# Kernel optimization log

Hardware: AMD Instinct MI355X
Metric: run time of the kernel (lower is better)

## Reference

```python
import jax, jax.numpy as jnp
import numpy as np

QMAX = 127.0          # int8 clip bound (symmetric, preserve-zero)
QDIV = 127.5          # AQT int8 scale divisor: 2**(bits-1) - 0.5


def _safe(s):
    # avoid div-by-zero for all-zero rows/cols
    return jnp.where(s == 0.0, 1.0, s)


def setup_inputs() -> dict:
    key = jax.random.key(0)
    k1, k2 = jax.random.split(key)
    lhs = jax.random.normal(k1, (8192, 4096), dtype=jnp.float32)
    rhs = jax.random.normal(k2, (4096, 4096), dtype=jnp.float32)
    return {"lhs": lhs, "rhs": rhs}


def reference(lhs, rhs):
    # --- dynamic symmetric int8 quantization (AQT abs-max calibration) ---
    # lhs: contract over axis 1 -> per-row scale [M, 1]
    s_l = _safe(jnp.max(jnp.abs(lhs), axis=1, keepdims=True) / QDIV)
    # rhs: contract over axis 0 -> per-column scale [1, N]
    s_r = _safe(jnp.max(jnp.abs(rhs), axis=0, keepdims=True) / QDIV)

    q_l = jnp.clip(jnp.round(lhs / s_l), -QMAX, QMAX).astype(jnp.int8)
    q_r = jnp.clip(jnp.round(rhs / s_r), -QMAX, QMAX).astype(jnp.int8)

    # --- integer matmul with int32 accumulation ---
    acc = jax.lax.dot_general(
        q_l, q_r,
        dimension_numbers=(((1,), (0,)), ((), ())),
        preferred_element_type=jnp.int32,
    )

    # --- dequantize: outer product of per-row / per-column scales ---
    return acc.astype(jnp.float32) * s_l * s_r
```

## Files before the change

kernel.cpp:

```cpp
#include <hip/hip_runtime.h>
#include <stdint.h>

#define M_DIM 8192
#define N_DIM 4096
#define K_DIM 4096
#define QMAXF 127.0f
#define QDIVF 127.5f

typedef int v4i __attribute__((ext_vector_type(4)));

typedef __attribute__((address_space(3))) void lds_void_t;
typedef __attribute__((address_space(1))) const void glb_void_t;

static __device__ __forceinline__ void load_lds16(const void* g, void* l) {
    __builtin_amdgcn_global_load_lds((glb_void_t*)g, (lds_void_t*)l, 16, 0, 0);
}

__global__ __launch_bounds__(256) void row_quant_kernel(
        const float* __restrict__ lhs, float* __restrict__ sL,
        int8_t* __restrict__ ql) {
    const int row = blockIdx.x;
    const float4* rp = (const float4*)(lhs + (size_t)row * K_DIM);
    const int t = threadIdx.x;
    float4 v[4];
    float m = 0.0f;
#pragma unroll
    for (int i = 0; i < 4; ++i) {
        v[i] = rp[t + i * 256];
        m = fmaxf(m, fmaxf(fmaxf(fabsf(v[i].x), fabsf(v[i].y)),
                           fmaxf(fabsf(v[i].z), fabsf(v[i].w))));
    }
#pragma unroll
    for (int off = 32; off; off >>= 1) m = fmaxf(m, __shfl_down(m, off, 64));
    __shared__ float wmax[4];
    if ((t & 63) == 0) wmax[t >> 6] = m;
    __syncthreads();
    const float mm = fmaxf(fmaxf(wmax[0], wmax[1]), fmaxf(wmax[2], wmax[3]));
    float s = mm / QDIVF;
    s = (s == 0.0f) ? 1.0f : s;
    if (t == 0) sL[row] = s;
    unsigned* qo = (unsigned*)ql + (size_t)row * 1024;
#pragma unroll
    for (int i = 0; i < 4; ++i) {
        int q0 = (int)fminf(fmaxf(rintf(v[i].x / s), -QMAXF), QMAXF);
        int q1 = (int)fminf(fmaxf(rintf(v[i].y / s), -QMAXF), QMAXF);
        int q2 = (int)fminf(fmaxf(rintf(v[i].z / s), -QMAXF), QMAXF);
        int q3 = (int)fminf(fmaxf(rintf(v[i].w / s), -QMAXF), QMAXF);
        qo[t + i * 256] = (q0 & 255) | ((q1 & 255) << 8) | ((q2 & 255) << 16)
                        | ((unsigned)(q3 & 255) << 24);
    }
}

__global__ __launch_bounds__(256) void col_absmax_kernel(
        const float* __restrict__ rhs, unsigned* __restrict__ bits) {
    const int col = blockIdx.x * 256 + threadIdx.x;
    const int r0 = blockIdx.y * 64;
    float m = 0.0f;
#pragma unroll 4
    for (int r = 0; r < 64; ++r)
        m = fmaxf(m, fabsf(rhs[(size_t)(r0 + r) * N_DIM + col]));
    atomicMax(&bits[col], __float_as_uint(m));
}

__global__ __launch_bounds__(256) void col_scale_kernel(
        const unsigned* __restrict__ bits, float* __restrict__ sR) {
    const int c = blockIdx.x * 256 + threadIdx.x;
    float s = __uint_as_float(bits[c]) / QDIVF;
    sR[c] = (s == 0.0f) ? 1.0f : s;
}

__global__ __launch_bounds__(256) void quant_rhs_t_kernel(
        const float* __restrict__ rhs, const float* __restrict__ sR,
        int8_t* __restrict__ qbT) {
    __shared__ __align__(16) int8_t lt[64][80];
    const int n0 = blockIdx.x * 64;
    const int k0 = blockIdx.y * 64;
    const int t = threadIdx.x;
    const int nloc = t & 63;
    const int kq = (t >> 6) * 16;
    const float s = sR[n0 + nloc];
#pragma unroll
    for (int i = 0; i < 4; ++i) {
        unsigned pack = 0;
#pragma unroll
        for (int j = 0; j < 4; ++j) {
            int kk = kq + i * 4 + j;
            float x = rhs[(size_t)(k0 + kk) * N_DIM + n0 + nloc];
            int q = (int)fminf(fmaxf(rintf(x / s), -QMAXF), QMAXF);
            pack |= (unsigned)(q & 255) << (8 * j);
        }
        *(unsigned*)&lt[nloc][kq + i * 4] = pack;
    }
    __syncthreads();
    const int nn = t >> 2, ch = t & 3;
    v4i val = *(const v4i*)&lt[nn][ch * 16];
    *(v4i*)&qbT[(size_t)(n0 + nn) * K_DIM + k0 + ch * 16] = val;
}


#define BAR() do { asm volatile("" ::: "memory");          \
                   __builtin_amdgcn_s_barrier();           \
                   asm volatile("" ::: "memory"); } while (0)

#define VMCNT(N) asm volatile("s_waitcnt vmcnt(%0)" :: "n"(N) : "memory")

#define STAGE_A(h, kt, bq) \
    load_lds16(gA0 + (size_t)((h) * 128) * K_DIM + (size_t)(kt) * 64, \
               lds + (bq) * 16384 + (h) * 8192 + sdst)
#define STAGE_B(h, kt, bq) \
    load_lds16(gB0 + (size_t)((h) * 128) * K_DIM + (size_t)(kt) * 64, \
               lds + 65536 + (bq) * 16384 + (h) * 8192 + sdst)

#define RD_A(BUF, MM) (*(const v4i*)(lds + (BUF) * 16384 + aoff[MM]))
#define RD_B(BUF, NN) (*(const v4i*)(lds + (BUF) * 16384 + boff[NN]))

#define TILE(KT, BUF, P, S, VM, RDN) do {                                       \
    _Pragma("unroll") for (int nn = 0; nn < 4; ++nn)                            \
        bfII[nn] = RD_B(BUF, 4 + nn);                                           \
    if (S) { STAGE_A(0, (KT) + 3, ((BUF) + 3) & 3);                             \
             STAGE_A(1, (KT) + 3, ((BUF) + 3) & 3);                             \
             STAGE_B(0, (KT) + 3, ((BUF) + 3) & 3);                             \
             STAGE_B(1, (KT) + 3, ((BUF) + 3) & 3); }                           \
    __builtin_amdgcn_s_setprio(1);                                              \
    _Pragma("unroll") for (int mm = 0; mm < 4; ++mm)                            \
    _Pragma("unroll") for (int nn = 0; nn < 4; ++nn)                            \
        acc[mm][nn] = __builtin_amdgcn_mfma_i32_16x16x64_i8(                    \
            af[P][mm], bfI[P][nn], acc[mm][nn], 0, 0, 0);                       \
    __builtin_amdgcn_s_setprio(0);                                              \
    if (RDN) {                                                                  \
        _Pragma("unroll") for (int mm = 0; mm < 4; ++mm)                        \
            af[(P) ^ 1][mm] = RD_A(((BUF) + 1) & 3, mm);                        \
        _Pragma("unroll") for (int nn = 0; nn < 4; ++nn)                        \
            bfI[(P) ^ 1][nn] = RD_B(((BUF) + 1) & 3, nn);                       \
    }                                                                           \
    __builtin_amdgcn_s_setprio(1);                                              \
    _Pragma("unroll") for (int mm = 0; mm < 4; ++mm)                            \
    _Pragma("unroll") for (int nn = 0; nn < 4; ++nn)                            \
        acc[mm][4 + nn] = __builtin_amdgcn_mfma_i32_16x16x64_i8(                \
            af[P][mm], bfII[nn], acc[mm][4 + nn], 0, 0, 0);                     \
    __builtin_amdgcn_s_setprio(0);                                              \
    VMCNT(VM);                                                                  \
    BAR();                                                                      \
} while (0)

__global__ __launch_bounds__(512, 2) void gemm_i8_kernel(
        const int8_t* __restrict__ qa, const int8_t* __restrict__ qbT,
        const float* __restrict__ sL, const float* __restrict__ sR,
        float* __restrict__ out) {
    __shared__ __align__(16) int8_t lds[131072];

    const int t = threadIdx.x;
    const int wave = t >> 6;
    const int lane = t & 63;

    const int bid = blockIdx.x;
    const int swz = (bid & 7) * 64 + (bid >> 3);
    const int brow = (swz & 31) * 256;
    const int bcol = (swz >> 5) * 256;

    const int wm = (wave >> 1) * 64;
    const int wn = (wave & 1) * 128;

    int aoff[4], boff[8];
#pragma unroll
    for (int m = 0; m < 4; ++m) {
        int row = wm + m * 16 + (lane & 15);
        aoff[m] = row * 64 + (((lane >> 4) ^ ((row >> 1) & 3)) * 16);
    }
#pragma unroll
    for (int n = 0; n < 8; ++n) {
        int row = wn + n * 16 + (lane & 15);
        boff[n] = 65536 + row * 64 + (((lane >> 4) ^ ((row >> 1) & 3)) * 16);
    }

    v4i acc[4][8];
#pragma unroll
    for (int m = 0; m < 4; ++m)
#pragma unroll
        for (int n = 0; n < 8; ++n) acc[m][n] = (v4i){0, 0, 0, 0};

    const int srow = t >> 2;
    const int lc = (t & 3) ^ ((srow >> 1) & 3);
    const int8_t* gA0 = qa  + (size_t)(brow + srow) * K_DIM + lc * 16;
    const int8_t* gB0 = qbT + (size_t)(bcol + srow) * K_DIM + lc * 16;
    const int sdst = t * 16;

    v4i af[2][4], bfI[2][4], bfII[4];

    STAGE_A(0, 0, 0); STAGE_A(1, 0, 0); STAGE_B(0, 0, 0); STAGE_B(1, 0, 0);
    STAGE_A(0, 1, 1); STAGE_A(1, 1, 1); STAGE_B(0, 1, 1); STAGE_B(1, 1, 1);
    STAGE_A(0, 2, 2); STAGE_A(1, 2, 2); STAGE_B(0, 2, 2); STAGE_B(1, 2, 2);
    VMCNT(4);
    BAR();
#pragma unroll
    for (int mm = 0; mm < 4; ++mm) af[0][mm] = RD_A(0, mm);
#pragma unroll
    for (int nn = 0; nn < 4; ++nn) bfI[0][nn] = RD_B(0, nn);

    for (int kt = 0; kt < 60; kt += 4) {
        TILE(kt + 0, 0, 0, 1, 4, 1);
        TILE(kt + 1, 1, 1, 1, 4, 1);
        TILE(kt + 2, 2, 0, 1, 4, 1);
        TILE(kt + 3, 3, 1, 1, 4, 1);
    }
    TILE(60, 0, 0, 1, 4, 1);
    TILE(61, 1, 1, 0, 0, 1);
    TILE(62, 2, 0, 0, 0, 1);
    TILE(63, 3, 1, 0, 0, 0);

    const int r4 = (lane >> 4) * 4;
    const int cc = lane & 15;
#pragma unroll
    for (int m = 0; m < 4; ++m) {
        const int grow0 = brow + wm + m * 16 + r4;
        const float s0 = sL[grow0 + 0];
        const float s1 = sL[grow0 + 1];
        const float s2 = sL[grow0 + 2];
        const float s3 = sL[grow0 + 3];
#pragma unroll
        for (int n = 0; n < 8; ++n) {
            const int gcol = bcol + wn + n * 16 + cc;
            const float sc = sR[gcol];
            float* o = out + (size_t)grow0 * N_DIM + gcol;
            o[0 * N_DIM] = (float)acc[m][n][0] * s0 * sc;
            o[1 * N_DIM] = (float)acc[m][n][1] * s1 * sc;
            o[2 * N_DIM] = (float)acc[m][n][2] * s2 * sc;
            o[3 * N_DIM] = (float)acc[m][n][3] * s3 * sc;
        }
    }
}

extern "C" void kernel_launch(void* const* d_in, const int* in_sizes, int n_in,
                              void* d_out, int out_size, void* d_ws, size_t ws_size,
                              hipStream_t stream) {
    const float* lhs = (const float*)d_in[0];
    const float* rhs = (const float*)d_in[1];
    float* out = (float*)d_out;

    uint8_t* ws = (uint8_t*)d_ws;
    int8_t* ql    = (int8_t*)ws;
    int8_t* qbT   = (int8_t*)(ws + 33554432);
    float* sL     = (float*)(ws + 50331648);
    float* sR     = (float*)(ws + 50331648 + 32768);
    unsigned* bits = (unsigned*)(ws + 50331648 + 32768 + 16384);

    hipMemsetAsync(bits, 0, N_DIM * sizeof(unsigned), stream);

    row_quant_kernel<<<M_DIM, 256, 0, stream>>>(lhs, sL, ql);
    col_absmax_kernel<<<dim3(N_DIM / 256, K_DIM / 64), 256, 0, stream>>>(rhs, bits);
    col_scale_kernel<<<N_DIM / 256, 256, 0, stream>>>(bits, sR);
    quant_rhs_t_kernel<<<dim3(N_DIM / 64, K_DIM / 64), 256, 0, stream>>>(rhs, sR, qbT);
    gemm_i8_kernel<<<dim3(M_DIM / 256 * N_DIM / 256), 512, 0, stream>>>(ql, qbT, sL, sR, out);
}
```

Before: 220.2 us.

## Shrink GEMM tile to 256x128 with double-buffered LDS and higher occupancy

Replaces the 256x256 block tile with a 4-stage LDS pipeline by a 256x128 tile using only two LDS buffers (48KB) and a simpler load-then-compute loop that waits for all loads each K step. Launch bounds are raised to allow four blocks per CU, and the XCD-aware block swizzle is rewritten for the new grid shape. The aim is to hide latency through occupancy rather than software pipelining. The smaller tile lowers arithmetic intensity and the full vmcnt(0) wait exposes global load latency each iteration.

```diff
diff --git a/kernel.cpp b/kernel.cpp
--- a/kernel.cpp
+++ b/kernel.cpp
@@ -104,109 +104,93 @@
 
 #define VMCNT(N) asm volatile("s_waitcnt vmcnt(%0)" :: "n"(N) : "memory")
 
-#define STAGE_A(h, kt, bq) \
-    load_lds16(gA0 + (size_t)((h) * 128) * K_DIM + (size_t)(kt) * 64, \
-               lds + (bq) * 16384 + (h) * 8192 + sdst)
-#define STAGE_B(h, kt, bq) \
-    load_lds16(gB0 + (size_t)((h) * 128) * K_DIM + (size_t)(kt) * 64, \
-               lds + 65536 + (bq) * 16384 + (h) * 8192 + sdst)
-
 #define RD_A(BUF, MM) (*(const v4i*)(lds + (BUF) * 16384 + aoff[MM]))
-#define RD_B(BUF, NN) (*(const v4i*)(lds + (BUF) * 16384 + boff[NN]))
-
-#define TILE(KT, BUF, P, S, VM, RDN) do {                                       \
-    _Pragma("unroll") for (int nn = 0; nn < 4; ++nn)                            \
-        bfII[nn] = RD_B(BUF, 4 + nn);                                           \
-    if (S) { STAGE_A(0, (KT) + 3, ((BUF) + 3) & 3);                             \
-             STAGE_A(1, (KT) + 3, ((BUF) + 3) & 3);                             \
-             STAGE_B(0, (KT) + 3, ((BUF) + 3) & 3);                             \
-             STAGE_B(1, (KT) + 3, ((BUF) + 3) & 3); }                           \
+#define RD_B(BUF, NN) (*(const v4i*)(lds + 32768 + (BUF) * 8192 + boff[NN]))
+
+#define TILE(BUF, S) do {                                                       \
+    if (S) {                                                                    \
+        load_lds16(pA,                      lds + ((BUF) ^ 1) * 16384 + sdst);  \
+        load_lds16(pA + (size_t)128 * K_DIM,                                    \
+                   lds + ((BUF) ^ 1) * 16384 + 8192 + sdst);                    \
+        load_lds16(pB, lds + 32768 + ((BUF) ^ 1) * 8192 + sdst);                \
+        pA += 64; pB += 64;                                                     \
+    }                                                                           \
+    _Pragma("unroll") for (int mm = 0; mm < 4; ++mm) af[mm] = RD_A(BUF, mm);    \
+    _Pragma("unroll") for (int nn = 0; nn < 4; ++nn) bf[nn] = RD_B(BUF, nn);    \
     __builtin_amdgcn_s_setprio(1);                                              \
     _Pragma("unroll") for (int mm = 0; mm < 4; ++mm)                            \
     _Pragma("unroll") for (int nn = 0; nn < 4; ++nn)                            \
         acc[mm][nn] = __builtin_amdgcn_mfma_i32_16x16x64_i8(                    \
-            af[P][mm], bfI[P][nn], acc[mm][nn], 0, 0, 0);                       \
+            af[mm], bf[nn], acc[mm][nn], 0, 0, 0);                              \
     __builtin_amdgcn_s_setprio(0);                                              \
-    if (RDN) {                                                                  \
-        _Pragma("unroll") for (int mm = 0; mm < 4; ++mm)                        \
-            af[(P) ^ 1][mm] = RD_A(((BUF) + 1) & 3, mm);                        \
-        _Pragma("unroll") for (int nn = 0; nn < 4; ++nn)                        \
-            bfI[(P) ^ 1][nn] = RD_B(((BUF) + 1) & 3, nn);                       \
-    }                                                                           \
-    __builtin_amdgcn_s_setprio(1);                                              \
-    _Pragma("unroll") for (int mm = 0; mm < 4; ++mm)                            \
-    _Pragma("unroll") for (int nn = 0; nn < 4; ++nn)                            \
-        acc[mm][4 + nn] = __builtin_amdgcn_mfma_i32_16x16x64_i8(                \
-            af[P][mm], bfII[nn], acc[mm][4 + nn], 0, 0, 0);                     \
-    __builtin_amdgcn_s_setprio(0);                                              \
-    VMCNT(VM);                                                                  \
+    VMCNT(0);                                                                   \
     BAR();                                                                      \
 } while (0)
 
-__global__ __launch_bounds__(512, 2) void gemm_i8_kernel(
+__global__ __launch_bounds__(512, 4) void gemm_i8_kernel(
         const int8_t* __restrict__ qa, const int8_t* __restrict__ qbT,
         const float* __restrict__ sL, const float* __restrict__ sR,
         float* __restrict__ out) {
-    __shared__ __align__(16) int8_t lds[131072];
+    __shared__ __align__(16) int8_t lds[49152];
 
     const int t = threadIdx.x;
     const int wave = t >> 6;
     const int lane = t & 63;
 
     const int bid = blockIdx.x;
-    const int swz = (bid & 7) * 64 + (bid >> 3);
-    const int brow = (swz & 31) * 256;
-    const int bcol = (swz >> 5) * 256;
+    const int xcd = bid & 7;
+    const int idx = bid >> 3;
+    const int mt = (xcd >> 1) * 8 + (idx & 7);
+    const int nt = (xcd & 1) * 16 + (idx >> 3);
+    const int brow = mt * 256;
+    const int bcol = nt * 128;
 
     const int wm = (wave >> 1) * 64;
-    const int wn = (wave & 1) * 128;
-
-    int aoff[4], boff[8];
+    const int wn = (wave & 1) * 64;
+
+    int aoff[4], boff[4];
 #pragma unroll
     for (int m = 0; m < 4; ++m) {
         int row = wm + m * 16 + (lane & 15);
         aoff[m] = row * 64 + (((lane >> 4) ^ ((row >> 1) & 3)) * 16);
     }
 #pragma unroll
-    for (int n = 0; n < 8; ++n) {
+    for (int n = 0; n < 4; ++n) {
         int row = wn + n * 16 + (lane & 15);
-        boff[n] = 65536 + row * 64 + (((lane >> 4) ^ ((row >> 1) & 3)) * 16);
-    }
-
-    v4i acc[4][8];
+        boff[n] = row * 64 + (((lane >> 4) ^ ((row >> 1) & 3)) * 16);
+    }
+
+    v4i acc[4][4];
 #pragma unroll
     for (int m = 0; m < 4; ++m)
 #pragma unroll
-        for (int n = 0; n < 8; ++n) acc[m][n] = (v4i){0, 0, 0, 0};
+        for (int n = 0; n < 4; ++n) acc[m][n] = (v4i){0, 0, 0, 0};
 
     const int srow = t >> 2;
-    const int lc = (t & 3) ^ ((srow >> 1) & 3);
-    const int8_t* gA0 = qa  + (size_t)(brow + srow) * K_DIM + lc * 16;
-    const int8_t* gB0 = qbT + (size_t)(bcol + srow) * K_DIM + lc * 16;
+    const int lc = (t & 3) ^ ((srow >> 3) & 3) ^ ((srow & 4) ? 0 : 0);
+    const int lcA = (t & 3) ^ ((srow >> 1) & 3);
+    (void)lc;
+    const int8_t* gA0 = qa  + (size_t)(brow + srow) * K_DIM + lcA * 16;
+    const int8_t* gB0 = qbT + (size_t)(bcol + srow) * K_DIM + lcA * 16;
     const int sdst = t * 16;
 
-    v4i af[2][4], bfI[2][4], bfII[4];
-
-    STAGE_A(0, 0, 0); STAGE_A(1, 0, 0); STAGE_B(0, 0, 0); STAGE_B(1, 0, 0);
-    STAGE_A(0, 1, 1); STAGE_A(1, 1, 1); STAGE_B(0, 1, 1); STAGE_B(1, 1, 1);
-    STAGE_A(0, 2, 2); STAGE_A(1, 2, 2); STAGE_B(0, 2, 2); STAGE_B(1, 2, 2);
-    VMCNT(4);
+    const int8_t* pA = gA0 + 64;
+    const int8_t* pB = gB0 + 64;
+
+    v4i af[4], bf[4];
+
+    load_lds16(gA0,                        lds + sdst);
+    load_lds16(gA0 + (size_t)128 * K_DIM,  lds + 8192 + sdst);
+    load_lds16(gB0,                        lds + 32768 + sdst);
+    VMCNT(0);
     BAR();
-#pragma unroll
-    for (int mm = 0; mm < 4; ++mm) af[0][mm] = RD_A(0, mm);
-#pragma unroll
-    for (int nn = 0; nn < 4; ++nn) bfI[0][nn] = RD_B(0, nn);
-
-    for (int kt = 0; kt < 60; kt += 4) {
-        TILE(kt + 0, 0, 0, 1, 4, 1);
-        TILE(kt + 1, 1, 1, 1, 4, 1);
-        TILE(kt + 2, 2, 0, 1, 4, 1);
-        TILE(kt + 3, 3, 1, 1, 4, 1);
-    }
-    TILE(60, 0, 0, 1, 4, 1);
-    TILE(61, 1, 1, 0, 0, 1);
-    TILE(62, 2, 0, 0, 0, 1);
-    TILE(63, 3, 1, 0, 0, 0);
+
+    for (int kt = 0; kt < 62; kt += 2) {
+        TILE(0, 1);
+        TILE(1, 1);
+    }
+    TILE(0, 1);
+    TILE(1, 0);
 
     const int r4 = (lane >> 4) * 4;
     const int cc = lane & 15;
@@ -218,7 +202,7 @@
         const float s2 = sL[grow0 + 2];
         const float s3 = sL[grow0 + 3];
 #pragma unroll
-        for (int n = 0; n < 8; ++n) {
+        for (int n = 0; n < 4; ++n) {
             const int gcol = bcol + wn + n * 16 + cc;
             const float sc = sR[gcol];
             float* o = out + (size_t)grow0 * N_DIM + gcol;
@@ -250,5 +234,6 @@
     col_absmax_kernel<<<dim3(N_DIM / 256, K_DIM / 64), 256, 0, stream>>>(rhs, bits);
     col_scale_kernel<<<N_DIM / 256, 256, 0, stream>>>(bits, sR);
     quant_rhs_t_kernel<<<dim3(N_DIM / 64, K_DIM / 64), 256, 0, stream>>>(rhs, sR, qbT);
-    gemm_i8_kernel<<<dim3(M_DIM / 256 * N_DIM / 256), 512, 0, stream>>>(ql, qbT, sL, sR, out);
-}
+    gemm_i8_kernel<<<dim3((M_DIM / 256) * (N_DIM / 128)), 512, 0, stream>>>(
+        ql, qbT, sL, sR, out);
+}
```

After: 233.0 us. +5.8%, slower.

## Fuse prep kernels into fewer launches and remap GEMM tiles per XCD

Applied to the files above, without the earlier changes.

Merges the row-quantization and column abs-max kernels into one launch with a block-index split, and folds the column-scale computation into the rhs transpose-quantize kernel. This removes two kernel launches and their serialization gaps. The GEMM block swizzle is also changed so each XCD handles an 8x8 patch of output tiles, which should improve L2 reuse of A and B within each die. The column abs-max now covers 128 rows per block instead of 64, which halves the atomics but gives each block more serial work.

```diff
diff --git a/kernel.cpp b/kernel.cpp
--- a/kernel.cpp
+++ b/kernel.cpp
@@ -16,69 +16,68 @@
     __builtin_amdgcn_global_load_lds((glb_void_t*)g, (lds_void_t*)l, 16, 0, 0);
 }
 
-__global__ __launch_bounds__(256) void row_quant_kernel(
-        const float* __restrict__ lhs, float* __restrict__ sL,
+__global__ __launch_bounds__(256) void prep1_kernel(
+        const float* __restrict__ lhs, const float* __restrict__ rhs,
+        float* __restrict__ sL, unsigned* __restrict__ bits,
         int8_t* __restrict__ ql) {
-    const int row = blockIdx.x;
-    const float4* rp = (const float4*)(lhs + (size_t)row * K_DIM);
     const int t = threadIdx.x;
-    float4 v[4];
-    float m = 0.0f;
-#pragma unroll
-    for (int i = 0; i < 4; ++i) {
-        v[i] = rp[t + i * 256];
-        m = fmaxf(m, fmaxf(fmaxf(fabsf(v[i].x), fabsf(v[i].y)),
-                           fmaxf(fabsf(v[i].z), fabsf(v[i].w))));
-    }
-#pragma unroll
-    for (int off = 32; off; off >>= 1) m = fmaxf(m, __shfl_down(m, off, 64));
-    __shared__ float wmax[4];
-    if ((t & 63) == 0) wmax[t >> 6] = m;
-    __syncthreads();
-    const float mm = fmaxf(fmaxf(wmax[0], wmax[1]), fmaxf(wmax[2], wmax[3]));
-    float s = mm / QDIVF;
-    s = (s == 0.0f) ? 1.0f : s;
-    if (t == 0) sL[row] = s;
-    unsigned* qo = (unsigned*)ql + (size_t)row * 1024;
-#pragma unroll
-    for (int i = 0; i < 4; ++i) {
-        int q0 = (int)fminf(fmaxf(rintf(v[i].x / s), -QMAXF), QMAXF);
-        int q1 = (int)fminf(fmaxf(rintf(v[i].y / s), -QMAXF), QMAXF);
-        int q2 = (int)fminf(fmaxf(rintf(v[i].z / s), -QMAXF), QMAXF);
-        int q3 = (int)fminf(fmaxf(rintf(v[i].w / s), -QMAXF), QMAXF);
-        qo[t + i * 256] = (q0 & 255) | ((q1 & 255) << 8) | ((q2 & 255) << 16)
-                        | ((unsigned)(q3 & 255) << 24);
-    }
-}
-
-__global__ __launch_bounds__(256) void col_absmax_kernel(
-        const float* __restrict__ rhs, unsigned* __restrict__ bits) {
-    const int col = blockIdx.x * 256 + threadIdx.x;
-    const int r0 = blockIdx.y * 64;
-    float m = 0.0f;
+    if (blockIdx.x < M_DIM) {
+        const int row = blockIdx.x;
+        const float4* rp = (const float4*)(lhs + (size_t)row * K_DIM);
+        float4 v[4];
+        float m = 0.0f;
+#pragma unroll
+        for (int i = 0; i < 4; ++i) {
+            v[i] = rp[t + i * 256];
+            m = fmaxf(m, fmaxf(fmaxf(fabsf(v[i].x), fabsf(v[i].y)),
+                               fmaxf(fabsf(v[i].z), fabsf(v[i].w))));
+        }
+#pragma unroll
+        for (int off = 32; off; off >>= 1) m = fmaxf(m, __shfl_down(m, off, 64));
+        __shared__ float wmax[4];
+        if ((t & 63) == 0) wmax[t >> 6] = m;
+        __syncthreads();
+        const float mm = fmaxf(fmaxf(wmax[0], wmax[1]), fmaxf(wmax[2], wmax[3]));
+        float s = mm / QDIVF;
+        s = (s == 0.0f) ? 1.0f : s;
+        if (t == 0) sL[row] = s;
+        unsigned* qo = (unsigned*)ql + (size_t)row * 1024;
+#pragma unroll
+        for (int i = 0; i < 4; ++i) {
+            int q0 = (int)fminf(fmaxf(rintf(v[i].x / s), -QMAXF), QMAXF);
+            int q1 = (int)fminf(fmaxf(rintf(v[i].y / s), -QMAXF), QMAXF);
+            int q2 = (int)fminf(fmaxf(rintf(v[i].z / s), -QMAXF), QMAXF);
+            int q3 = (int)fminf(fmaxf(rintf(v[i].w / s), -QMAXF), QMAXF);
+            qo[t + i * 256] = (q0 & 255) | ((q1 & 255) << 8) | ((q2 & 255) << 16)
+                            | ((unsigned)(q3 & 255) << 24);
+        }
+    } else {
+        const int cb = blockIdx.x - M_DIM;
+        const int col = (cb & 15) * 256 + t;
+        const int r0 = (cb >> 4) * 128;
+        float m = 0.0f;
 #pragma unroll 4
-    for (int r = 0; r < 64; ++r)
-        m = fmaxf(m, fabsf(rhs[(size_t)(r0 + r) * N_DIM + col]));
-    atomicMax(&bits[col], __float_as_uint(m));
-}
-
-__global__ __launch_bounds__(256) void col_scale_kernel(
-        const unsigned* __restrict__ bits, float* __restrict__ sR) {
-    const int c = blockIdx.x * 256 + threadIdx.x;
-    float s = __uint_as_float(bits[c]) / QDIVF;
-    sR[c] = (s == 0.0f) ? 1.0f : s;
+        for (int r = 0; r < 128; ++r)
+            m = fmaxf(m, fabsf(rhs[(size_t)(r0 + r) * N_DIM + col]));
+        atomicMax(&bits[col], __float_as_uint(m));
+    }
 }
 
 __global__ __launch_bounds__(256) void quant_rhs_t_kernel(
-        const float* __restrict__ rhs, const float* __restrict__ sR,
-        int8_t* __restrict__ qbT) {
+        const float* __restrict__ rhs, const unsigned* __restrict__ bits,
+        float* __restrict__ sR, int8_t* __restrict__ qbT) {
     __shared__ __align__(16) int8_t lt[64][80];
     const int n0 = blockIdx.x * 64;
     const int k0 = blockIdx.y * 64;
     const int t = threadIdx.x;
     const int nloc = t & 63;
     const int kq = (t >> 6) * 16;
-    const float s = sR[n0 + nloc];
+    float s = __uint_as_float(bits[n0 + nloc]) / QDIVF;
+    s = (s == 0.0f) ? 1.0f : s;
+    if (blockIdx.y == 0 && t < 64) {
+        float ss = __uint_as_float(bits[n0 + t]) / QDIVF;
+        sR[n0 + t] = (ss == 0.0f) ? 1.0f : ss;
+    }
 #pragma unroll
     for (int i = 0; i < 4; ++i) {
         unsigned pack = 0;
@@ -154,9 +153,12 @@
     const int lane = t & 63;
 
     const int bid = blockIdx.x;
-    const int swz = (bid & 7) * 64 + (bid >> 3);
-    const int brow = (swz & 31) * 256;
-    const int bcol = (swz >> 5) * 256;
+    const int xcd = bid & 7;
+    const int idx = bid >> 3;
+    const int mt = (xcd >> 1) * 8 + (idx & 7);
+    const int nt = (xcd & 1) * 8 + (idx >> 3);
+    const int brow = mt * 256;
+    const int bcol = nt * 256;
 
     const int wm = (wave >> 1) * 64;
     const int wn = (wave & 1) * 128;
@@ -180,9 +182,9 @@
         for (int n = 0; n < 8; ++n) acc[m][n] = (v4i){0, 0, 0, 0};
 
     const int srow = t >> 2;
-    const int lc = (t & 3) ^ ((srow >> 1) & 3);
-    const int8_t* gA0 = qa  + (size_t)(brow + srow) * K_DIM + lc * 16;
-    const int8_t* gB0 = qbT + (size_t)(bcol + srow) * K_DIM + lc * 16;
+    const int lcA = (t & 3) ^ ((srow >> 1) & 3);
+    const int8_t* gA0 = qa  + (size_t)(brow + srow) * K_DIM + lcA * 16;
+    const int8_t* gB0 = qbT + (size_t)(bcol + srow) * K_DIM + lcA * 16;
     const int sdst = t * 16;
 
     v4i af[2][4], bfI[2][4], bfII[4];
@@ -246,9 +248,9 @@
 
     hipMemsetAsync(bits, 0, N_DIM * sizeof(unsigned), stream);
 
-    row_quant_kernel<<<M_DIM, 256, 0, stream>>>(lhs, sL, ql);
-    col_absmax_kernel<<<dim3(N_DIM / 256, K_DIM / 64), 256, 0, stream>>>(rhs, bits);
-    col_scale_kernel<<<N_DIM / 256, 256, 0, stream>>>(bits, sR);
-    quant_rhs_t_kernel<<<dim3(N_DIM / 64, K_DIM / 64), 256, 0, stream>>>(rhs, sR, qbT);
-    gemm_i8_kernel<<<dim3(M_DIM / 256 * N_DIM / 256), 512, 0, stream>>>(ql, qbT, sL, sR, out);
-}
+    prep1_kernel<<<M_DIM + 512, 256, 0, stream>>>(lhs, rhs, sL, bits, ql);
+    quant_rhs_t_kernel<<<dim3(N_DIM / 64, K_DIM / 64), 256, 0, stream>>>(
+        rhs, bits, sR, qbT);
+    gemm_i8_kernel<<<dim3((M_DIM / 256) * (N_DIM / 256)), 512, 0, stream>>>(
+        ql, qbT, sL, sR, out);
+}
```

Result: slower. 230.4 us (+4.6%).
